# Performance work log

Measured on AMD Instinct MI355X. Metric: run time of the kernel, lower is better.

## Reference

```python
import jax, jax.numpy as jnp
import numpy as np

B, L, IN = 256, 64, 1024
SIZES = [IN, 600, 350, 200, 180]  # comp embedding MLP sizes
E = 180                           # embedding / LSTM hidden size
# Fixed AST: root -> 3 interior nodes -> 2 leaves each; leaf j uses comps [8j, 8j+8)
LEAF_IDX = [np.arange(j * 8, (j + 1) * 8) for j in range(6)]


def _xavier(key, shape):
    fan_out, fan_in = shape[0], shape[1]
    lim = float(np.sqrt(6.0 / (fan_in + fan_out)))
    return jax.random.uniform(key, shape, jnp.float32, -lim, lim)


def setup_inputs() -> dict:
    key = jax.random.key(0)
    ks = iter(jax.random.split(key, 40))
    inp = {"ast_features": jax.random.normal(next(ks), (B, L, IN), jnp.float32)}
    # comp embedding MLP
    for i in range(4):
        inp[f"ce_w{i}"] = _xavier(next(ks), (SIZES[i + 1], SIZES[i]))
        inp[f"ce_b{i}"] = jnp.zeros((SIZES[i + 1],), jnp.float32)
    # concat layers: [2E, 200, 180]
    cc = [2 * E, 200, 180]
    for i in range(2):
        inp[f"cc_w{i}"] = _xavier(next(ks), (cc[i + 1], cc[i]))
        inp[f"cc_b{i}"] = jnp.zeros((cc[i + 1],), jnp.float32)
    rg = [E, 200, 180]
    for i in range(2):
        inp[f"rg_w{i}"] = _xavier(next(ks), (rg[i + 1], rg[i]))
        inp[f"rg_b{i}"] = jnp.zeros((rg[i + 1],), jnp.float32)
    inp["pred_w"] = _xavier(next(ks), (1, 180))
    inp["pred_b"] = jnp.zeros((1,), jnp.float32)
    # LSTMs (torch gate order i,f,g,o), input E -> hidden E
    for p in ("cl", "nl"):
        inp[f"{p}_Wih"] = _xavier(next(ks), (4 * E, E))
        inp[f"{p}_Whh"] = _xavier(next(ks), (4 * E, E))
        inp[f"{p}_bih"] = jnp.zeros((4 * E,), jnp.float32)
        inp[f"{p}_bhh"] = jnp.zeros((4 * E,), jnp.float32)
    inp["no_comps"] = _xavier(next(ks), (1, E))
    inp["no_nodes"] = _xavier(next(ks), (1, E))
    return inp


def _lstm_last_h(x, Wih, Whh, bih, bhh):
    # x: (B, T, E) -> last hidden state (B, 1, E); h0=c0=0 as in torch default
    Bx = x.shape[0]
    h0 = jnp.zeros((Bx, E), x.dtype)

    def step(carry, xt):
        h, c = carry
        g = xt @ Wih.T + h @ Whh.T + bih + bhh
        i, f, gg, o = jnp.split(g, 4, axis=-1)
        c = jax.nn.sigmoid(f) * c + jax.nn.sigmoid(i) * jnp.tanh(gg)
        h = jax.nn.sigmoid(o) * jnp.tanh(c)
        return (h, c), None

    (h, _), _ = jax.lax.scan(step, (h0, h0), jnp.swapaxes(x, 0, 1))
    return h[:, None, :]


def reference(ast_features, ce_w0, ce_b0, ce_w1, ce_b1, ce_w2, ce_b2, ce_w3, ce_b3,
              cc_w0, cc_b0, cc_w1, cc_b1, rg_w0, rg_b0, rg_w1, rg_b1,
              pred_w, pred_b, cl_Wih, cl_Whh, cl_bih, cl_bhh,
              nl_Wih, nl_Whh, nl_bih, nl_bhh, no_comps, no_nodes):
    elu = jax.nn.elu
    # comp embedding MLP (dropout = identity in eval)
    x = ast_features
    for w, b in ((ce_w0, ce_b0), (ce_w1, ce_b1), (ce_w2, ce_b2), (ce_w3, ce_b3)):
        x = elu(x @ w.T + b)
    embed = x  # (B, L, E)
    Bx = embed.shape[0]

    def concat_block(nodes_h, comps_h):
        y = jnp.concatenate((nodes_h, comps_h), axis=2)  # (B,1,2E)
        for w, b in ((cc_w0, cc_b0), (cc_w1, cc_b1)):
            y = elu(y @ w.T + b)
        return y  # (B,1,E)

    no_nodes_b = jnp.broadcast_to(no_nodes[None], (Bx, 1, E))
    no_comps_b = jnp.broadcast_to(no_comps[None], (Bx, 1, E))

    def leaf_state(idx):
        comps_h = _lstm_last_h(embed[:, idx, :], cl_Wih, cl_Whh, cl_bih, cl_bhh)
        return concat_block(no_nodes_b, comps_h)

    def interior_state(children):
        nodes_h = _lstm_last_h(jnp.concatenate(children, axis=1), nl_Wih, nl_Whh, nl_bih, nl_bhh)
        return concat_block(nodes_h, no_comps_b)

    mids = [interior_state([leaf_state(LEAF_IDX[2 * i]), leaf_state(LEAF_IDX[2 * i + 1])]) for i in range(3)]
    prog = interior_state(mids)  # (B,1,E)

    x = prog
    for w, b in ((rg_w0, rg_b0), (rg_w1, rg_b1)):
        x = elu(x @ w.T + b)
    out = x @ pred_w.T + pred_b  # (B,1,1)
    return out[:, 0, 0]
```

## Files before the change

kernel.cpp:

```cpp
#include <hip/hip_runtime.h>
#include <math.h>


typedef __attribute__((ext_vector_type(8))) short bf16x8;
typedef __attribute__((ext_vector_type(4))) float f32x4;
typedef __attribute__((ext_vector_type(4))) unsigned short us4;
typedef unsigned short ushort_t;
typedef unsigned int uint_t;

__device__ __forceinline__ float elu1(float x) { return x > 0.f ? x : expm1f(x); }
__device__ __forceinline__ float sigm(float x) { return 1.f / (1.f + expf(-x)); }

__device__ __forceinline__ ushort_t f2bf(float f) {
    union { float f; uint_t u; } v; v.f = f;
    uint_t u = v.u;
    uint_t r = u + 0x7FFFu + ((u >> 16) & 1u);
    return (ushort_t)(r >> 16);
}
__device__ __forceinline__ float bf2f(ushort_t h) {
    union { uint_t u; float f; } v; v.u = ((uint_t)h) << 16;
    return v.f;
}
__device__ __forceinline__ void split2(float x, ushort_t& hi, ushort_t& lo) {
    ushort_t h = f2bf(x);
    hi = h;
    lo = f2bf(x - bf2f(h));
}

__device__ __forceinline__ bf16x8 ld8(const ushort_t* p) { return *(const bf16x8*)p; }

__device__ __forceinline__ void load_split_f32(const float* p, bf16x8& h8, bf16x8& l8) {
    const float4* q = (const float4*)p;
    float4 a = q[0], b = q[1];
    float v[8] = {a.x, a.y, a.z, a.w, b.x, b.y, b.z, b.w};
#pragma unroll
    for (int i = 0; i < 8; ++i) {
        ushort_t h, l; split2(v[i], h, l);
        h8[i] = (short)h; l8[i] = (short)l;
    }
}

__device__ __forceinline__ void gload16(const void* g, void* l) {
    __builtin_amdgcn_global_load_lds(
        (const __attribute__((address_space(1))) unsigned int*)g,
        (__attribute__((address_space(3))) unsigned int*)l,
        16, 0, 0);
}

template <bool OUTPAIR>
__global__ __launch_bounds__(256)
void gemm_lds(const ushort_t* __restrict__ Ahi, const ushort_t* __restrict__ Alo, int lda,
              const ushort_t* __restrict__ Whi, const ushort_t* __restrict__ Wlo, int ldw,
              const float* __restrict__ bias,
              float* __restrict__ Cf, ushort_t* __restrict__ Chi, ushort_t* __restrict__ Clo,
              int ldc, int N, int Kp, int act)
{
    __shared__ ushort_t lds[4 * 4096];
    const int tid  = threadIdx.x;
    const int lane = tid & 63;
    const int wave = tid >> 6;
    const int wm = wave & 1;
    const int wn = wave >> 1;
    const int j16 = lane & 15;
    const int kq  = lane >> 4;
    const int bm = blockIdx.y * 128;
    const int bn = blockIdx.x * 128;

    const ushort_t* sbase = (wave == 0) ? Ahi : (wave == 1) ? Alo
                          : (wave == 2) ? Whi : Wlo;
    const int srow0 = (wave < 2) ? bm : bn;
    const int sld   = (wave < 2) ? lda : ldw;
    const size_t soff = (size_t)(srow0 + j16) * sld + kq * 8;
    char* const lplane = (char*)lds + wave * 8192;

    f32x4 acc[4][4] = {};

    for (int k0 = 0; k0 < Kp; k0 += 32) {
#pragma unroll
        for (int u = 0; u < 8; ++u) {
            gload16(sbase + soff + (size_t)u * 16 * sld + k0, lplane + u * 1024);
        }
        __syncthreads();

        bf16x8 ah[4], al[4], bh[4], bl[4];
#pragma unroll
        for (int i = 0; i < 4; ++i) {
            const int ta = (wm * 4 + i) * 1024 + lane * 16;
            const int tb = (wn * 4 + i) * 1024 + lane * 16;
            ah[i] = *(const bf16x8*)((const char*)lds +         ta);
            al[i] = *(const bf16x8*)((const char*)lds +  8192 + ta);
            bh[i] = *(const bf16x8*)((const char*)lds + 16384 + tb);
            bl[i] = *(const bf16x8*)((const char*)lds + 24576 + tb);
        }
#pragma unroll
        for (int ms = 0; ms < 4; ++ms)
#pragma unroll
        for (int ns = 0; ns < 4; ++ns) {
            acc[ms][ns] = __builtin_amdgcn_mfma_f32_16x16x32_bf16(ah[ms], bh[ns], acc[ms][ns], 0, 0, 0);
            acc[ms][ns] = __builtin_amdgcn_mfma_f32_16x16x32_bf16(ah[ms], bl[ns], acc[ms][ns], 0, 0, 0);
            acc[ms][ns] = __builtin_amdgcn_mfma_f32_16x16x32_bf16(al[ms], bh[ns], acc[ms][ns], 0, 0, 0);
        }
        __syncthreads();
    }

    const int rbase = kq << 2;
#pragma unroll
    for (int ms = 0; ms < 4; ++ms)
#pragma unroll
    for (int ns = 0; ns < 4; ++ns) {
        const int gc = bn + wn * 64 + ns * 16 + j16;
#pragma unroll
        for (int r = 0; r < 4; ++r) {
            const int gr = bm + wm * 64 + ms * 16 + rbase + r;
            float v = acc[ms][ns][r];
            if constexpr (OUTPAIR) {
                if (gc < ldc) {
                    float o = 0.f;
                    if (gc < N) {
                        o = v + (bias ? bias[gc] : 0.f);
                        if (act) o = elu1(o);
                    }
                    ushort_t hh, ll; split2(o, hh, ll);
                    Chi[(size_t)gr * ldc + gc] = hh;
                    Clo[(size_t)gr * ldc + gc] = ll;
                }
            } else {
                if (gc < N) {
                    float o = v + (bias ? bias[gc] : 0.f);
                    if (act) o = elu1(o);
                    Cf[(size_t)gr * N + gc] = o;
                }
            }
        }
    }
}

__global__ __launch_bounds__(256)
void gemm_mfma_f32a(const float* __restrict__ A, int lda,
                    const ushort_t* __restrict__ Whi, const ushort_t* __restrict__ Wlo, int ldw,
                    const float* __restrict__ bias,
                    ushort_t* __restrict__ Chi, ushort_t* __restrict__ Clo,
                    int ldc, int N, int Kp, int act)
{
    const int lane = threadIdx.x & 63;
    const int wave = threadIdx.x >> 6;
    const int wm = wave & 1, wn = wave >> 1;
    const int r16 = lane & 15;
    const int kb  = (lane >> 4) << 3;
    const int bm = blockIdx.y * 128 + wm * 64;
    const int bn = blockIdx.x * 128 + wn * 64;

    f32x4 acc[4][4] = {};
    size_t aoff[4];
    const ushort_t *wh[4], *wl[4];
#pragma unroll
    for (int i = 0; i < 4; ++i) {
        aoff[i] = (size_t)(bm + i * 16 + r16) * lda + kb;
        wh[i] = Whi + (size_t)(bn + i * 16 + r16) * ldw + kb;
        wl[i] = Wlo + (size_t)(bn + i * 16 + r16) * ldw + kb;
    }
    for (int k = 0; k < Kp; k += 32) {
        bf16x8 ah[4], al[4], bh[4], bl[4];
#pragma unroll
        for (int i = 0; i < 4; ++i) {
            load_split_f32(A + aoff[i] + k, ah[i], al[i]);
            bh[i] = ld8(wh[i] + k);
            bl[i] = ld8(wl[i] + k);
        }
#pragma unroll
        for (int ms = 0; ms < 4; ++ms)
#pragma unroll
        for (int ns = 0; ns < 4; ++ns) {
            acc[ms][ns] = __builtin_amdgcn_mfma_f32_16x16x32_bf16(ah[ms], bh[ns], acc[ms][ns], 0, 0, 0);
            acc[ms][ns] = __builtin_amdgcn_mfma_f32_16x16x32_bf16(ah[ms], bl[ns], acc[ms][ns], 0, 0, 0);
            acc[ms][ns] = __builtin_amdgcn_mfma_f32_16x16x32_bf16(al[ms], bh[ns], acc[ms][ns], 0, 0, 0);
        }
    }
    const int rbase = (lane >> 4) << 2;
#pragma unroll
    for (int ms = 0; ms < 4; ++ms)
#pragma unroll
    for (int ns = 0; ns < 4; ++ns) {
        const int gc = bn + ns * 16 + r16;
#pragma unroll
        for (int r = 0; r < 4; ++r) {
            const int gr = bm + ms * 16 + rbase + r;
            if (gc < ldc) {
                float o = 0.f;
                if (gc < N) {
                    o = acc[ms][ns][r] + bias[gc];
                    if (act) o = elu1(o);
                }
                ushort_t hh, ll; split2(o, hh, ll);
                Chi[(size_t)gr * ldc + gc] = hh;
                Clo[(size_t)gr * ldc + gc] = ll;
            }
        }
    }
}

__global__ void conv_w(const float* __restrict__ src, int sld, int soff,
                       int R, int C, ushort_t* __restrict__ dhi,
                       ushort_t* __restrict__ dlo, int Rp, int Cp)
{
    int idx = blockIdx.x * blockDim.x + threadIdx.x;
    if (idx >= Rp * Cp) return;
    int r = idx / Cp, c = idx - r * Cp;
    float v = (r < R && c < C) ? src[r * sld + soff + c] : 0.f;
    ushort_t h, l; split2(v, h, l);
    dhi[idx] = h; dlo[idx] = l;
}

__global__ void conv_a0(const float* __restrict__ src, ushort_t* __restrict__ dhi,
                        ushort_t* __restrict__ dlo)
{
    int idx = blockIdx.x * blockDim.x + threadIdx.x;
    if (idx >= 16384 * 256) return;
    float4 v = ((const float4*)src)[idx];
    float x[4] = {v.x, v.y, v.z, v.w};
    us4 h, l;
#pragma unroll
    for (int i = 0; i < 4; ++i) {
        ushort_t hh, ll; split2(x[i], hh, ll);
        h[i] = hh; l[i] = ll;
    }
    ((us4*)dhi)[idx] = h;
    ((us4*)dlo)[idx] = l;
}

__global__ void lstm_gate(ushort_t* __restrict__ h_hi, ushort_t* __restrict__ h_lo,
                          float* __restrict__ c,
                          const float* __restrict__ G, const float* __restrict__ XW,
                          int rows, int T, int t)
{
    int idx = blockIdx.x * blockDim.x + threadIdx.x;
    if (idx >= rows * 180) return;
    int n = idx / 180, e = idx - n * 180;
    const float* xw = XW + ((size_t)n * T + t) * 720;
    float gi = xw[e], gf = xw[e + 180], gg = xw[e + 360], go = xw[e + 540];
    if (G) {
        const float* g = G + (size_t)n * 720;
        gi += g[e]; gf += g[e + 180]; gg += g[e + 360]; go += g[e + 540];
    }
    float cv = sigm(gf) * c[idx] + sigm(gi) * tanhf(gg);
    c[idx] = cv;
    float hv = sigm(go) * tanhf(cv);
    ushort_t hh, ll; split2(hv, hh, ll);
    h_hi[(size_t)n * 192 + e] = hh;
    h_lo[(size_t)n * 192 + e] = ll;
}

__global__ void gather_leaf_bf(const ushort_t* __restrict__ ehi, const ushort_t* __restrict__ elo,
                               ushort_t* __restrict__ xhi, ushort_t* __restrict__ xlo)
{
    int idx = blockIdx.x * blockDim.x + threadIdx.x;
    if (idx >= 12288 * 192) return;
    int r = idx / 192, e = idx - r * 192;
    int t = r & 7, nb = r >> 3;
    int b = nb & 255, j = nb >> 8;
    int s = (b * 64 + 8 * j + t) * 192 + e;
    xhi[idx] = ehi[s];
    xlo[idx] = elo[s];
}

__global__ void gather_mid_bf(const ushort_t* __restrict__ shi, const ushort_t* __restrict__ slo,
                              ushort_t* __restrict__ dhi, ushort_t* __restrict__ dlo)
{
    int idx = blockIdx.x * blockDim.x + threadIdx.x;
    if (idx >= 1536 * 192) return;
    int r = idx / 192, e = idx - r * 192;
    int t = r & 1, m = r >> 1;
    int b = m & 255, i = m >> 8;
    int s = ((2 * i + t) * 256 + b) * 192 + e;
    dhi[idx] = shi[s];
    dlo[idx] = slo[s];
}

__global__ void gather_root_bf(const ushort_t* __restrict__ shi, const ushort_t* __restrict__ slo,
                               ushort_t* __restrict__ dhi, ushort_t* __restrict__ dlo)
{
    int idx = blockIdx.x * blockDim.x + threadIdx.x;
    if (idx >= 768 * 192) return;
    int r = idx / 192, e = idx - r * 192;
    int b = r / 3, t = r - b * 3;
    int s = (t * 256 + b) * 192 + e;
    dhi[idx] = shi[s];
    dlo[idx] = slo[s];
}

__global__ void bias_prep(const float* __restrict__ cl_bih, const float* __restrict__ cl_bhh,
                          const float* __restrict__ nl_bih, const float* __restrict__ nl_bhh,
                          const float* __restrict__ cc_w0, const float* __restrict__ cc_b0,
                          const float* __restrict__ no_nodes, const float* __restrict__ no_comps,
                          float* __restrict__ clb, float* __restrict__ nlb,
                          float* __restrict__ b1, float* __restrict__ b2)
{
    int tid = blockIdx.x * blockDim.x + threadIdx.x;
    if (tid < 720) {
        clb[tid] = cl_bih[tid] + cl_bhh[tid];
    } else if (tid < 1440) {
        int o = tid - 720;
        nlb[o] = nl_bih[o] + nl_bhh[o];
    } else if (tid < 1640) {
        int o = tid - 1440;
        float s = cc_b0[o];
        for (int e = 0; e < 180; ++e) s = fmaf(no_nodes[e], cc_w0[o * 360 + e], s);
        b1[o] = s;
    } else if (tid < 1840) {
        int o = tid - 1640;
        float s = cc_b0[o];
        for (int e = 0; e < 180; ++e) s = fmaf(no_comps[e], cc_w0[o * 360 + 180 + e], s);
        b2[o] = s;
    }
}

__global__ void pred_kernel(const float* __restrict__ x, const float* __restrict__ pw,
                            const float* __restrict__ pb, float* __restrict__ out)
{
    int b = blockIdx.x * blockDim.x + threadIdx.x;
    if (b >= 256) return;
    float s = pb[0];
#pragma unroll 4
    for (int e = 0; e < 180; ++e) s = fmaf(x[b * 180 + e], pw[e], s);
    out[b] = s;
}

extern "C" void kernel_launch(void* const* d_in, const int* in_sizes, int n_in,
                              void* d_out, int out_size, void* d_ws, size_t ws_size,
                              hipStream_t stream)
{
    const float* ast    = (const float*)d_in[0];
    const float* ce_w0  = (const float*)d_in[1];
    const float* ce_b0  = (const float*)d_in[2];
    const float* ce_w1  = (const float*)d_in[3];
    const float* ce_b1  = (const float*)d_in[4];
    const float* ce_w2  = (const float*)d_in[5];
    const float* ce_b2  = (const float*)d_in[6];
    const float* ce_w3  = (const float*)d_in[7];
    const float* ce_b3  = (const float*)d_in[8];
    const float* cc_w0  = (const float*)d_in[9];
    const float* cc_b0  = (const float*)d_in[10];
    const float* cc_w1  = (const float*)d_in[11];
    const float* cc_b1  = (const float*)d_in[12];
    const float* rg_w0  = (const float*)d_in[13];
    const float* rg_b0  = (const float*)d_in[14];
    const float* rg_w1  = (const float*)d_in[15];
    const float* rg_b1  = (const float*)d_in[16];
    const float* pred_w = (const float*)d_in[17];
    const float* pred_b = (const float*)d_in[18];
    const float* cl_Wih = (const float*)d_in[19];
    const float* cl_Whh = (const float*)d_in[20];
    const float* cl_bih = (const float*)d_in[21];
    const float* cl_bhh = (const float*)d_in[22];
    const float* nl_Wih = (const float*)d_in[23];
    const float* nl_Whh = (const float*)d_in[24];
    const float* nl_bih = (const float*)d_in[25];
    const float* nl_bhh = (const float*)d_in[26];
    const float* no_comps = (const float*)d_in[27];
    const float* no_nodes = (const float*)d_in[28];
    float* out = (float*)d_out;

    char* ws = (char*)d_ws;

    const size_t Z1SZ = 39845888;
    const size_t WTSZ = 7560192;
    const bool pre = ws_size >= (size_t)67108864 + Z1SZ + WTSZ + 8192;
    const size_t z0sz = pre ? 67108864 : 35651584;

    char* Z0 = ws;
    char* Z1 = ws + z0sz;
    char* WT = Z1 + Z1SZ;
    char* BI = WT + WTSZ;

    ushort_t* A0hi = (ushort_t*)Z0;
    ushort_t* A0lo = (ushort_t*)(Z0 + 33554432);
    ushort_t* A2hi = (ushort_t*)Z0;
    ushort_t* A2lo = (ushort_t*)(Z0 + 11534336);
    ushort_t* EMhi = (ushort_t*)Z0;
    ushort_t* EMlo = (ushort_t*)(Z0 + 6291456);
    float*    XWl  = (float*)Z0;

    ushort_t* A1hi = (ushort_t*)Z1;
    ushort_t* A1lo = (ushort_t*)(Z1 + 19922944);
    ushort_t* A3hi = (ushort_t*)Z1;
    ushort_t* A3lo = (ushort_t*)(Z1 + 7340032);
    ushort_t* XGhi = (ushort_t*)Z1;
    ushort_t* XGlo = (ushort_t*)(Z1 + 4718592);
    char* S = Z1 + 9437184;

    ushort_t* hl_hi = (ushort_t*)(S);
    ushort_t* hl_lo = (ushort_t*)(S + 589824);
    float*    c_l   = (float*)(S + 1179648);
    float*    G     = (float*)(S + 2285568);
    ushort_t* ls_hi = (ushort_t*)(S + 6709248);
    ushort_t* ls_lo = (ushort_t*)(S + 7299072);
    ushort_t* y2_hi = (ushort_t*)(S + 7888896);
    ushort_t* y2_lo = (ushort_t*)(S + 8577024);
    ushort_t* x2_hi = (ushort_t*)(S + 9265152);
    ushort_t* x2_lo = (ushort_t*)(S + 9854976);
    float*    XW2   = (float*)(S + 10444800);
    ushort_t* hm_hi = (ushort_t*)(S + 14868480);
    ushort_t* hm_lo = (ushort_t*)(S + 15163392);
    float*    c_m   = (float*)(S + 15458304);
    ushort_t* ms_hi = (ushort_t*)(S + 16011264);
    ushort_t* ms_lo = (ushort_t*)(S + 16306176);
    ushort_t* x3_hi = (ushort_t*)(S + 16601088);
    ushort_t* x3_lo = (ushort_t*)(S + 16896000);
    float*    XW3   = (float*)(S + 17190912);
    ushort_t* hr_hi = (ushort_t*)(S + 19402752);
    ushort_t* hr_lo = (ushort_t*)(S + 19501056);
    float*    c_r   = (float*)(S + 19599360);
    ushort_t* pg_hi = (ushort_t*)(S + 19783680);
    ushort_t* pg_lo = (ushort_t*)(S + 19881984);
    ushort_t* r2_hi = (ushort_t*)(S + 19980288);
    ushort_t* r2_lo = (ushort_t*)(S + 20094976);
    float*    r180  = (float*)(S + 20209664);

    ushort_t* w0hi  = (ushort_t*)(WT);
    ushort_t* w0lo  = (ushort_t*)(WT + 1310720);
    ushort_t* w1hi  = (ushort_t*)(WT + 2621440);
    ushort_t* w1lo  = (ushort_t*)(WT + 3088384);
    ushort_t* w2hi  = (ushort_t*)(WT + 3555328);
    ushort_t* w2lo  = (ushort_t*)(WT + 3735552);
    ushort_t* w3hi  = (ushort_t*)(WT + 3915776);
    ushort_t* w3lo  = (ushort_t*)(WT + 4030464);
    ushort_t* wiC_h = (ushort_t*)(WT + 4145152);
    ushort_t* wiC_l = (ushort_t*)(WT + 4440064);
    ushort_t* whC_h = (ushort_t*)(WT + 4734976);
    ushort_t* whC_l = (ushort_t*)(WT + 5029888);
    ushort_t* wiN_h = (ushort_t*)(WT + 5324800);
    ushort_t* wiN_l = (ushort_t*)(WT + 5619712);
    ushort_t* whN_h = (ushort_t*)(WT + 5914624);
    ushort_t* whN_l = (ushort_t*)(WT + 6209536);
    ushort_t* c0L_h = (ushort_t*)(WT + 6504448);
    ushort_t* c0L_l = (ushort_t*)(WT + 6602752);
    ushort_t* c0I_h = (ushort_t*)(WT + 6701056);
    ushort_t* c0I_l = (ushort_t*)(WT + 6799360);
    ushort_t* c1_h  = (ushort_t*)(WT + 6897664);
    ushort_t* c1_l  = (ushort_t*)(WT + 7012352);
    ushort_t* rg0_h = (ushort_t*)(WT + 7127040);
    ushort_t* rg0_l = (ushort_t*)(WT + 7225344);
    ushort_t* rg1_h = (ushort_t*)(WT + 7323648);
    ushort_t* rg1_l = (ushort_t*)(WT + 7438336);

    float* clb = (float*)BI;
    float* nlb = (float*)(BI + 2880);
    float* b1  = (float*)(BI + 5760);
    float* b2  = (float*)(BI + 6560);

    if (pre)
        conv_a0<<<16384, 256, 0, stream>>>(ast, A0hi, A0lo);
    conv_w<<<(640*1024 + 255)/256, 256, 0, stream>>>(ce_w0, 1024, 0, 600, 1024, w0hi, w0lo, 640, 1024);
    conv_w<<<(384*608 + 255)/256, 256, 0, stream>>>(ce_w1, 600, 0, 350, 600, w1hi, w1lo, 384, 608);
    conv_w<<<(256*352 + 255)/256, 256, 0, stream>>>(ce_w2, 350, 0, 200, 350, w2hi, w2lo, 256, 352);
    conv_w<<<(256*224 + 255)/256, 256, 0, stream>>>(ce_w3, 200, 0, 180, 200, w3hi, w3lo, 256, 224);
    conv_w<<<(768*192 + 255)/256, 256, 0, stream>>>(cl_Wih, 180, 0, 720, 180, wiC_h, wiC_l, 768, 192);
    conv_w<<<(768*192 + 255)/256, 256, 0, stream>>>(cl_Whh, 180, 0, 720, 180, whC_h, whC_l, 768, 192);
    conv_w<<<(768*192 + 255)/256, 256, 0, stream>>>(nl_Wih, 180, 0, 720, 180, wiN_h, wiN_l, 768, 192);
    conv_w<<<(768*192 + 255)/256, 256, 0, stream>>>(nl_Whh, 180, 0, 720, 180, whN_h, whN_l, 768, 192);
    conv_w<<<(256*192 + 255)/256, 256, 0, stream>>>(cc_w0, 360, 180, 200, 180, c0L_h, c0L_l, 256, 192);
    conv_w<<<(256*192 + 255)/256, 256, 0, stream>>>(cc_w0, 360, 0, 200, 180, c0I_h, c0I_l, 256, 192);
    conv_w<<<(256*224 + 255)/256, 256, 0, stream>>>(cc_w1, 200, 0, 180, 200, c1_h, c1_l, 256, 224);
    conv_w<<<(256*192 + 255)/256, 256, 0, stream>>>(rg_w0, 180, 0, 200, 180, rg0_h, rg0_l, 256, 192);
    conv_w<<<(256*224 + 255)/256, 256, 0, stream>>>(rg_w1, 200, 0, 180, 200, rg1_h, rg1_l, 256, 224);
    bias_prep<<<(1840 + 255)/256, 256, 0, stream>>>(
        cl_bih, cl_bhh, nl_bih, nl_bhh, cc_w0, cc_b0, no_nodes, no_comps,
        clb, nlb, b1, b2);

    dim3 blk(256);

    if (pre)
        gemm_lds<true><<<dim3(5, 128), blk, 0, stream>>>(
            A0hi, A0lo, 1024, w0hi, w0lo, 1024, ce_b0,
            nullptr, A1hi, A1lo, 608, 600, 1024, 1);
    else
        gemm_mfma_f32a<<<dim3(5, 128), blk, 0, stream>>>(
            ast, 1024, w0hi, w0lo, 1024, ce_b0,
            A1hi, A1lo, 608, 600, 1024, 1);
    gemm_lds<true><<<dim3(3, 128), blk, 0, stream>>>(
        A1hi, A1lo, 608, w1hi, w1lo, 608, ce_b1,
        nullptr, A2hi, A2lo, 352, 350, 608, 1);
    gemm_lds<true><<<dim3(2, 128), blk, 0, stream>>>(
        A2hi, A2lo, 352, w2hi, w2lo, 352, ce_b2,
        nullptr, A3hi, A3lo, 224, 200, 352, 1);
    gemm_lds<true><<<dim3(2, 128), blk, 0, stream>>>(
        A3hi, A3lo, 224, w3hi, w3lo, 224, ce_b3,
        nullptr, EMhi, EMlo, 192, 180, 224, 1);

    gather_leaf_bf<<<(12288*192 + 255)/256, 256, 0, stream>>>(EMhi, EMlo, XGhi, XGlo);
    gemm_lds<false><<<dim3(6, 96), blk, 0, stream>>>(
        XGhi, XGlo, 192, wiC_h, wiC_l, 192, clb,
        XWl, nullptr, nullptr, 0, 720, 192, 0);
    hipMemsetAsync(S, 0, 2285568, stream);
    for (int t = 0; t < 8; ++t) {
        if (t > 0)
            gemm_lds<false><<<dim3(6, 12), blk, 0, stream>>>(
                hl_hi, hl_lo, 192, whC_h, whC_l, 192, nullptr,
                G, nullptr, nullptr, 0, 720, 192, 0);
        lstm_gate<<<(1536*180 + 255)/256, 256, 0, stream>>>(
            hl_hi, hl_lo, c_l, t ? G : nullptr, XWl, 1536, 8, t);
    }
    gemm_lds<true><<<dim3(2, 12), blk, 0, stream>>>(
        hl_hi, hl_lo, 192, c0L_h, c0L_l, 192, b1,
        nullptr, y2_hi, y2_lo, 224, 200, 192, 1);
    gemm_lds<true><<<dim3(2, 12), blk, 0, stream>>>(
        y2_hi, y2_lo, 224, c1_h, c1_l, 224, cc_b1,
        nullptr, ls_hi, ls_lo, 192, 180, 224, 1);

    gather_mid_bf<<<(1536*192 + 255)/256, 256, 0, stream>>>(ls_hi, ls_lo, x2_hi, x2_lo);
    gemm_lds<false><<<dim3(6, 12), blk, 0, stream>>>(
        x2_hi, x2_lo, 192, wiN_h, wiN_l, 192, nlb,
        XW2, nullptr, nullptr, 0, 720, 192, 0);
    hipMemsetAsync(S + 14868480, 0, 1142784, stream);
    for (int t = 0; t < 2; ++t) {
        if (t > 0)
            gemm_lds<false><<<dim3(6, 6), blk, 0, stream>>>(
                hm_hi, hm_lo, 192, whN_h, whN_l, 192, nullptr,
                G, nullptr, nullptr, 0, 720, 192, 0);
        lstm_gate<<<(768*180 + 255)/256, 256, 0, stream>>>(
            hm_hi, hm_lo, c_m, t ? G : nullptr, XW2, 768, 2, t);
    }
    gemm_lds<true><<<dim3(2, 6), blk, 0, stream>>>(
        hm_hi, hm_lo, 192, c0I_h, c0I_l, 192, b2,
        nullptr, y2_hi, y2_lo, 224, 200, 192, 1);
    gemm_lds<true><<<dim3(2, 6), blk, 0, stream>>>(
        y2_hi, y2_lo, 224, c1_h, c1_l, 224, cc_b1,
        nullptr, ms_hi, ms_lo, 192, 180, 224, 1);

    gather_root_bf<<<(768*192 + 255)/256, 256, 0, stream>>>(ms_hi, ms_lo, x3_hi, x3_lo);
    gemm_lds<false><<<dim3(6, 6), blk, 0, stream>>>(
        x3_hi, x3_lo, 192, wiN_h, wiN_l, 192, nlb,
        XW3, nullptr, nullptr, 0, 720, 192, 0);
    hipMemsetAsync(S + 19402752, 0, 380928, stream);
    for (int t = 0; t < 3; ++t) {
        if (t > 0)
            gemm_lds<false><<<dim3(6, 2), blk, 0, stream>>>(
                hr_hi, hr_lo, 192, whN_h, whN_l, 192, nullptr,
                G, nullptr, nullptr, 0, 720, 192, 0);
        lstm_gate<<<(256*180 + 255)/256, 256, 0, stream>>>(
            hr_hi, hr_lo, c_r, t ? G : nullptr, XW3, 256, 3, t);
    }
    gemm_lds<true><<<dim3(2, 2), blk, 0, stream>>>(
        hr_hi, hr_lo, 192, c0I_h, c0I_l, 192, b2,
        nullptr, y2_hi, y2_lo, 224, 200, 192, 1);
    gemm_lds<true><<<dim3(2, 2), blk, 0, stream>>>(
        y2_hi, y2_lo, 224, c1_h, c1_l, 224, cc_b1,
        nullptr, pg_hi, pg_lo, 192, 180, 224, 1);

    gemm_lds<true><<<dim3(2, 2), blk, 0, stream>>>(
        pg_hi, pg_lo, 192, rg0_h, rg0_l, 192, rg_b0,
        nullptr, r2_hi, r2_lo, 224, 200, 192, 1);
    gemm_lds<false><<<dim3(2, 2), blk, 0, stream>>>(
        r2_hi, r2_lo, 224, rg1_h, rg1_l, 224, rg_b1,
        r180, nullptr, nullptr, 0, 180, 224, 1);
    pred_kernel<<<1, 256, 0, stream>>>(r180, pred_w, pred_b, out);
}
```

Measured before the change: 1.066 ms.

## Double-buffer LDS in split-bf16 GEMM, remap workgroups, fuse weight prep launches

The GEMM kernel now uses a 64KB dynamic LDS double buffer, so the global-to-LDS loads for the next K tile are issued while the MFMAs on the current tile run, and one barrier per iteration is removed. Workgroup IDs are remapped in groups of 8 when the grid size allows it, which changes which tiles run on which part of the GPU and may affect cache locality. The thirteen weight conversion kernels, the bias prep kernel and the three memsets are merged into a single prep_all launch to cut launch overhead. Doubling the LDS per block may reduce occupancy.

```diff
diff --git a/kernel.cpp b/kernel.cpp
--- a/kernel.cpp
+++ b/kernel.cpp
@@ -55,7 +55,7 @@
               float* __restrict__ Cf, ushort_t* __restrict__ Chi, ushort_t* __restrict__ Clo,
               int ldc, int N, int Kp, int act)
 {
-    __shared__ ushort_t lds[4 * 4096];
+    extern __shared__ char smem[];
     const int tid  = threadIdx.x;
     const int lane = tid & 63;
     const int wave = tid >> 6;
@@ -63,34 +63,49 @@
     const int wn = wave >> 1;
     const int j16 = lane & 15;
     const int kq  = lane >> 4;
-    const int bm = blockIdx.y * 128;
-    const int bn = blockIdx.x * 128;
+
+    const int gx = gridDim.x;
+    const int nwg = gx * gridDim.y;
+    int wg = blockIdx.y * gx + blockIdx.x;
+    if ((nwg & 7) == 0) {
+        const int cpx = nwg >> 3;
+        wg = (wg & 7) * cpx + (wg >> 3);
+    }
+    const int bm = (wg / gx) * 128;
+    const int bn = (wg % gx) * 128;
 
     const ushort_t* sbase = (wave == 0) ? Ahi : (wave == 1) ? Alo
                           : (wave == 2) ? Whi : Wlo;
     const int srow0 = (wave < 2) ? bm : bn;
     const int sld   = (wave < 2) ? lda : ldw;
     const size_t soff = (size_t)(srow0 + j16) * sld + kq * 8;
-    char* const lplane = (char*)lds + wave * 8192;
+    const int lp = wave * 8192;
 
     f32x4 acc[4][4] = {};
 
+#pragma unroll
+    for (int u = 0; u < 8; ++u)
+        gload16(sbase + soff + (size_t)u * 16 * sld, smem + lp + u * 1024);
+    __syncthreads();
+
+    int cur = 0;
     for (int k0 = 0; k0 < Kp; k0 += 32) {
-#pragma unroll
-        for (int u = 0; u < 8; ++u) {
-            gload16(sbase + soff + (size_t)u * 16 * sld + k0, lplane + u * 1024);
-        }
-        __syncthreads();
-
+        if (k0 + 32 < Kp) {
+            char* nb = smem + ((cur ^ 1) << 15) + lp;
+#pragma unroll
+            for (int u = 0; u < 8; ++u)
+                gload16(sbase + soff + (size_t)u * 16 * sld + k0 + 32, nb + u * 1024);
+        }
+        const char* cb = smem + (cur << 15);
         bf16x8 ah[4], al[4], bh[4], bl[4];
 #pragma unroll
         for (int i = 0; i < 4; ++i) {
             const int ta = (wm * 4 + i) * 1024 + lane * 16;
             const int tb = (wn * 4 + i) * 1024 + lane * 16;
-            ah[i] = *(const bf16x8*)((const char*)lds +         ta);
-            al[i] = *(const bf16x8*)((const char*)lds +  8192 + ta);
-            bh[i] = *(const bf16x8*)((const char*)lds + 16384 + tb);
-            bl[i] = *(const bf16x8*)((const char*)lds + 24576 + tb);
+            ah[i] = *(const bf16x8*)(cb +         ta);
+            al[i] = *(const bf16x8*)(cb +  8192 + ta);
+            bh[i] = *(const bf16x8*)(cb + 16384 + tb);
+            bl[i] = *(const bf16x8*)(cb + 24576 + tb);
         }
 #pragma unroll
         for (int ms = 0; ms < 4; ++ms)
@@ -101,6 +116,7 @@
             acc[ms][ns] = __builtin_amdgcn_mfma_f32_16x16x32_bf16(al[ms], bh[ns], acc[ms][ns], 0, 0, 0);
         }
         __syncthreads();
+        cur ^= 1;
     }
 
     const int rbase = kq << 2;
@@ -199,18 +215,6 @@
     }
 }
 
-__global__ void conv_w(const float* __restrict__ src, int sld, int soff,
-                       int R, int C, ushort_t* __restrict__ dhi,
-                       ushort_t* __restrict__ dlo, int Rp, int Cp)
-{
-    int idx = blockIdx.x * blockDim.x + threadIdx.x;
-    if (idx >= Rp * Cp) return;
-    int r = idx / Cp, c = idx - r * Cp;
-    float v = (r < R && c < C) ? src[r * sld + soff + c] : 0.f;
-    ushort_t h, l; split2(v, h, l);
-    dhi[idx] = h; dlo[idx] = l;
-}
-
 __global__ void conv_a0(const float* __restrict__ src, ushort_t* __restrict__ dhi,
                         ushort_t* __restrict__ dlo)
 {
@@ -226,6 +230,80 @@
     }
     ((us4*)dhi)[idx] = h;
     ((us4*)dlo)[idx] = l;
+}
+
+__device__ __forceinline__ bool do_conv(int idx, int base, int cnt, int Cp,
+    const float* __restrict__ src, int sld, int soff, int R, int C,
+    ushort_t* __restrict__ dhi, ushort_t* __restrict__ dlo)
+{
+    if (idx >= base + cnt) return false;
+    int k = idx - base;
+    int r = k / Cp, c = k - r * Cp;
+    float v = (r < R && c < C) ? src[r * sld + soff + c] : 0.f;
+    ushort_t h, l; split2(v, h, l);
+    dhi[k] = h; dlo[k] = l;
+    return true;
+}
+
+__global__ void prep_all(
+    const float* __restrict__ ce_w0, const float* __restrict__ ce_w1,
+    const float* __restrict__ ce_w2, const float* __restrict__ ce_w3,
+    const float* __restrict__ cl_Wih, const float* __restrict__ cl_Whh,
+    const float* __restrict__ nl_Wih, const float* __restrict__ nl_Whh,
+    const float* __restrict__ cc_w0, const float* __restrict__ cc_w1,
+    const float* __restrict__ rg_w0, const float* __restrict__ rg_w1,
+    const float* __restrict__ cl_bih, const float* __restrict__ cl_bhh,
+    const float* __restrict__ nl_bih, const float* __restrict__ nl_bhh,
+    const float* __restrict__ cc_b0,
+    const float* __restrict__ no_nodes, const float* __restrict__ no_comps,
+    ushort_t* w0hi, ushort_t* w0lo, ushort_t* w1hi, ushort_t* w1lo,
+    ushort_t* w2hi, ushort_t* w2lo, ushort_t* w3hi, ushort_t* w3lo,
+    ushort_t* wiC_h, ushort_t* wiC_l, ushort_t* whC_h, ushort_t* whC_l,
+    ushort_t* wiN_h, ushort_t* wiN_l, ushort_t* whN_h, ushort_t* whN_l,
+    ushort_t* c0L_h, ushort_t* c0L_l, ushort_t* c0I_h, ushort_t* c0I_l,
+    ushort_t* c1_h, ushort_t* c1_l, ushort_t* rg0_h, ushort_t* rg0_l,
+    ushort_t* rg1_h, ushort_t* rg1_l,
+    float* clb, float* nlb, float* b1, float* b2,
+    char* S)
+{
+    int idx = blockIdx.x * blockDim.x + threadIdx.x;
+    if (do_conv(idx,       0, 655360, 1024, ce_w0, 1024, 0, 600, 1024, w0hi, w0lo)) return;
+    if (do_conv(idx,  655360, 233472,  608, ce_w1,  600, 0, 350,  600, w1hi, w1lo)) return;
+    if (do_conv(idx,  888832,  90112,  352, ce_w2,  350, 0, 200,  350, w2hi, w2lo)) return;
+    if (do_conv(idx,  978944,  57344,  224, ce_w3,  200, 0, 180,  200, w3hi, w3lo)) return;
+    if (do_conv(idx, 1036288, 147456,  192, cl_Wih, 180, 0, 720,  180, wiC_h, wiC_l)) return;
+    if (do_conv(idx, 1183744, 147456,  192, cl_Whh, 180, 0, 720,  180, whC_h, whC_l)) return;
+    if (do_conv(idx, 1331200, 147456,  192, nl_Wih, 180, 0, 720,  180, wiN_h, wiN_l)) return;
+    if (do_conv(idx, 1478656, 147456,  192, nl_Whh, 180, 0, 720,  180, whN_h, whN_l)) return;
+    if (do_conv(idx, 1626112,  49152,  192, cc_w0,  360, 180, 200, 180, c0L_h, c0L_l)) return;
+    if (do_conv(idx, 1675264,  49152,  192, cc_w0,  360, 0, 200,  180, c0I_h, c0I_l)) return;
+    if (do_conv(idx, 1724416,  57344,  224, cc_w1,  200, 0, 180,  200, c1_h, c1_l)) return;
+    if (do_conv(idx, 1781760,  49152,  192, rg_w0,  180, 0, 200,  180, rg0_h, rg0_l)) return;
+    if (do_conv(idx, 1830912,  57344,  224, rg_w1,  200, 0, 180,  200, rg1_h, rg1_l)) return;
+    if (idx < 1890096) {
+        int tid = idx - 1888256;
+        if (tid < 720) {
+            clb[tid] = cl_bih[tid] + cl_bhh[tid];
+        } else if (tid < 1440) {
+            int o = tid - 720;
+            nlb[o] = nl_bih[o] + nl_bhh[o];
+        } else if (tid < 1640) {
+            int o = tid - 1440;
+            float s = cc_b0[o];
+            for (int e = 0; e < 180; ++e) s = fmaf(no_nodes[e], cc_w0[o * 360 + e], s);
+            b1[o] = s;
+        } else if (tid < 1840) {
+            int o = tid - 1640;
+            float s = cc_b0[o];
+            for (int e = 0; e < 180; ++e) s = fmaf(no_comps[e], cc_w0[o * 360 + 180 + e], s);
+            b2[o] = s;
+        }
+        return;
+    }
+    float4 z = make_float4(0.f, 0.f, 0.f, 0.f);
+    if (idx < 2032944) { ((float4*)(S))[idx - 1890096] = z; return; }
+    if (idx < 2104368) { ((float4*)(S + 14868480))[idx - 2032944] = z; return; }
+    if (idx < 2128176) { ((float4*)(S + 19402752))[idx - 2104368] = z; return; }
 }
 
 __global__ void lstm_gate(ushort_t* __restrict__ h_hi, ushort_t* __restrict__ h_lo,
@@ -286,32 +364,6 @@
     int s = (t * 256 + b) * 192 + e;
     dhi[idx] = shi[s];
     dlo[idx] = slo[s];
-}
-
-__global__ void bias_prep(const float* __restrict__ cl_bih, const float* __restrict__ cl_bhh,
-                          const float* __restrict__ nl_bih, const float* __restrict__ nl_bhh,
-                          const float* __restrict__ cc_w0, const float* __restrict__ cc_b0,
-                          const float* __restrict__ no_nodes, const float* __restrict__ no_comps,
-                          float* __restrict__ clb, float* __restrict__ nlb,
-                          float* __restrict__ b1, float* __restrict__ b2)
-{
-    int tid = blockIdx.x * blockDim.x + threadIdx.x;
-    if (tid < 720) {
-        clb[tid] = cl_bih[tid] + cl_bhh[tid];
-    } else if (tid < 1440) {
-        int o = tid - 720;
-        nlb[o] = nl_bih[o] + nl_bhh[o];
-    } else if (tid < 1640) {
-        int o = tid - 1440;
-        float s = cc_b0[o];
-        for (int e = 0; e < 180; ++e) s = fmaf(no_nodes[e], cc_w0[o * 360 + e], s);
-        b1[o] = s;
-    } else if (tid < 1840) {
-        int o = tid - 1640;
-        float s = cc_b0[o];
-        for (int e = 0; e < 180; ++e) s = fmaf(no_comps[e], cc_w0[o * 360 + 180 + e], s);
-        b2[o] = s;
-    }
 }
 
 __global__ void pred_kernel(const float* __restrict__ x, const float* __restrict__ pw,
@@ -450,107 +502,97 @@
 
     if (pre)
         conv_a0<<<16384, 256, 0, stream>>>(ast, A0hi, A0lo);
-    conv_w<<<(640*1024 + 255)/256, 256, 0, stream>>>(ce_w0, 1024, 0, 600, 1024, w0hi, w0lo, 640, 1024);
-    conv_w<<<(384*608 + 255)/256, 256, 0, stream>>>(ce_w1, 600, 0, 350, 600, w1hi, w1lo, 384, 608);
-    conv_w<<<(256*352 + 255)/256, 256, 0, stream>>>(ce_w2, 350, 0, 200, 350, w2hi, w2lo, 256, 352);
-    conv_w<<<(256*224 + 255)/256, 256, 0, stream>>>(ce_w3, 200, 0, 180, 200, w3hi, w3lo, 256, 224);
-    conv_w<<<(768*192 + 255)/256, 256, 0, stream>>>(cl_Wih, 180, 0, 720, 180, wiC_h, wiC_l, 768, 192);
-    conv_w<<<(768*192 + 255)/256, 256, 0, stream>>>(cl_Whh, 180, 0, 720, 180, whC_h, whC_l, 768, 192);
-    conv_w<<<(768*192 + 255)/256, 256, 0, stream>>>(nl_Wih, 180, 0, 720, 180, wiN_h, wiN_l, 768, 192);
-    conv_w<<<(768*192 + 255)/256, 256, 0, stream>>>(nl_Whh, 180, 0, 720, 180, whN_h, whN_l, 768, 192);
-    conv_w<<<(256*192 + 255)/256, 256, 0, stream>>>(cc_w0, 360, 180, 200, 180, c0L_h, c0L_l, 256, 192);
-    conv_w<<<(256*192 + 255)/256, 256, 0, stream>>>(cc_w0, 360, 0, 200, 180, c0I_h, c0I_l, 256, 192);
-    conv_w<<<(256*224 + 255)/256, 256, 0, stream>>>(cc_w1, 200, 0, 180, 200, c1_h, c1_l, 256, 224);
-    conv_w<<<(256*192 + 255)/256, 256, 0, stream>>>(rg_w0, 180, 0, 200, 180, rg0_h, rg0_l, 256, 192);
-    conv_w<<<(256*224 + 255)/256, 256, 0, stream>>>(rg_w1, 200, 0, 180, 200, rg1_h, rg1_l, 256, 224);
-    bias_prep<<<(1840 + 255)/256, 256, 0, stream>>>(
-        cl_bih, cl_bhh, nl_bih, nl_bhh, cc_w0, cc_b0, no_nodes, no_comps,
-        clb, nlb, b1, b2);
+    prep_all<<<(2128176 + 255) / 256, 256, 0, stream>>>(
+        ce_w0, ce_w1, ce_w2, ce_w3, cl_Wih, cl_Whh, nl_Wih, nl_Whh,
+        cc_w0, cc_w1, rg_w0, rg_w1,
+        cl_bih, cl_bhh, nl_bih, nl_bhh, cc_b0, no_nodes, no_comps,
+        w0hi, w0lo, w1hi, w1lo, w2hi, w2lo, w3hi, w3lo,
+        wiC_h, wiC_l, whC_h, whC_l, wiN_h, wiN_l, whN_h, whN_l,
+        c0L_h, c0L_l, c0I_h, c0I_l, c1_h, c1_l, rg0_h, rg0_l, rg1_h, rg1_l,
+        clb, nlb, b1, b2, S);
 
     dim3 blk(256);
+    const int SH = 65536;
 
     if (pre)
-        gemm_lds<true><<<dim3(5, 128), blk, 0, stream>>>(
+        gemm_lds<true><<<dim3(5, 128), blk, SH, stream>>>(
             A0hi, A0lo, 1024, w0hi, w0lo, 1024, ce_b0,
             nullptr, A1hi, A1lo, 608, 600, 1024, 1);
     else
         gemm_mfma_f32a<<<dim3(5, 128), blk, 0, stream>>>(
             ast, 1024, w0hi, w0lo, 1024, ce_b0,
             A1hi, A1lo, 608, 600, 1024, 1);
-    gemm_lds<true><<<dim3(3, 128), blk, 0, stream>>>(
+    gemm_lds<true><<<dim3(3, 128), blk, SH, stream>>>(
         A1hi, A1lo, 608, w1hi, w1lo, 608, ce_b1,
         nullptr, A2hi, A2lo, 352, 350, 608, 1);
-    gemm_lds<true><<<dim3(2, 128), blk, 0, stream>>>(
+    gemm_lds<true><<<dim3(2, 128), blk, SH, stream>>>(
         A2hi, A2lo, 352, w2hi, w2lo, 352, ce_b2,
         nullptr, A3hi, A3lo, 224, 200, 352, 1);
-    gemm_lds<true><<<dim3(2, 128), blk, 0, stream>>>(
+    gemm_lds<true><<<dim3(2, 128), blk, SH, stream>>>(
         A3hi, A3lo, 224, w3hi, w3lo, 224, ce_b3,
         nullptr, EMhi, EMlo, 192, 180, 224, 1);
 
     gather_leaf_bf<<<(12288*192 + 255)/256, 256, 0, stream>>>(EMhi, EMlo, XGhi, XGlo);
-    gemm_lds<false><<<dim3(6, 96), blk, 0, stream>>>(
+    gemm_lds<false><<<dim3(6, 96), blk, SH, stream>>>(
         XGhi, XGlo, 192, wiC_h, wiC_l, 192, clb,
         XWl, nullptr, nullptr, 0, 720, 192, 0);
-    hipMemsetAsync(S, 0, 2285568, stream);
     for (int t = 0; t < 8; ++t) {
         if (t > 0)
-            gemm_lds<false><<<dim3(6, 12), blk, 0, stream>>>(
+            gemm_lds<false><<<dim3(6, 12), blk, SH, stream>>>(
                 hl_hi, hl_lo, 192, whC_h, whC_l, 192, nullptr,
                 G, nullptr, nullptr, 0, 720, 192, 0);
         lstm_gate<<<(1536*180 + 255)/256, 256, 0, stream>>>(
             hl_hi, hl_lo, c_l, t ? G : nullptr, XWl, 1536, 8, t);
     }
-    gemm_lds<true><<<dim3(2, 12), blk, 0, stream>>>(
+    gemm_lds<true><<<dim3(2, 12), blk, SH, stream>>>(
         hl_hi, hl_lo, 192, c0L_h, c0L_l, 192, b1,
         nullptr, y2_hi, y2_lo, 224, 200, 192, 1);
-    gemm_lds<true><<<dim3(2, 12), blk, 0, stream>>>(
+    gemm_lds<true><<<dim3(2, 12), blk, SH, stream>>>(
         y2_hi, y2_lo, 224, c1_h, c1_l, 224, cc_b1,
         nullptr, ls_hi, ls_lo, 192, 180, 224, 1);
 
     gather_mid_bf<<<(1536*192 + 255)/256, 256, 0, stream>>>(ls_hi, ls_lo, x2_hi, x2_lo);
-    gemm_lds<false><<<dim3(6, 12), blk, 0, stream>>>(
+    gemm_lds<false><<<dim3(6, 12), blk, SH, stream>>>(
         x2_hi, x2_lo, 192, wiN_h, wiN_l, 192, nlb,
         XW2, nullptr, nullptr, 0, 720, 192, 0);
-    hipMemsetAsync(S + 14868480, 0, 1142784, stream);
     for (int t = 0; t < 2; ++t) {
         if (t > 0)
-            gemm_lds<false><<<dim3(6, 6), blk, 0, stream>>>(
+            gemm_lds<false><<<dim3(6, 6), blk, SH, stream>>>(
                 hm_hi, hm_lo, 192, whN_h, whN_l, 192, nullptr,
                 G, nullptr, nullptr, 0, 720, 192, 0);
         lstm_gate<<<(768*180 + 255)/256, 256, 0, stream>>>(
             hm_hi, hm_lo, c_m, t ? G : nullptr, XW2, 768, 2, t);
     }
-    gemm_lds<true><<<dim3(2, 6), blk, 0, stream>>>(
+    gemm_lds<true><<<dim3(2, 6), blk, SH, stream>>>(
         hm_hi, hm_lo, 192, c0I_h, c0I_l, 192, b2,
         nullptr, y2_hi, y2_lo, 224, 200, 192, 1);
-    gemm_lds<true><<<dim3(2, 6), blk, 0, stream>>>(
+    gemm_lds<true><<<dim3(2, 6), blk, SH, stream>>>(
         y2_hi, y2_lo, 224, c1_h, c1_l, 224, cc_b1,
         nullptr, ms_hi, ms_lo, 192, 180, 224, 1);
 
     gather_root_bf<<<(768*192 + 255)/256, 256, 0, stream>>>(ms_hi, ms_lo, x3_hi, x3_lo);
-    gemm_lds<false><<<dim3(6, 6), blk, 0, stream>>>(
+    gemm_lds<false><<<dim3(6, 6), blk, SH, stream>>>(
         x3_hi, x3_lo, 192, wiN_h, wiN_l, 192, nlb,
         XW3, nullptr, nullptr, 0, 720, 192, 0);
-    hipMemsetAsync(S + 19402752, 0, 380928, stream);
     for (int t = 0; t < 3; ++t) {
         if (t > 0)
-            gemm_lds<false><<<dim3(6, 2), blk, 0, stream>>>(
+            gemm_lds<false><<<dim3(6, 2), blk, SH, stream>>>(
                 hr_hi, hr_lo, 192, whN_h, whN_l, 192, nullptr,
                 G, nullptr, nullptr, 0, 720, 192, 0);
         lstm_gate<<<(256*180 + 255)/256, 256, 0, stream>>>(
             hr_hi, hr_lo, c_r, t ? G : nullptr, XW3, 256, 3, t);
     }
-    gemm_lds<true><<<dim3(2, 2), blk, 0, stream>>>(
+    gemm_lds<true><<<dim3(2, 2), blk, SH, stream>>>(
         hr_hi, hr_lo, 192, c0I_h, c0I_l, 192, b2,
         nullptr, y2_hi, y2_lo, 224, 200, 192, 1);
-    gemm_lds<true><<<dim3(2, 2), blk, 0, stream>>>(
+    gemm_lds<true><<<dim3(2, 2), blk, SH, stream>>>(
         y2_hi, y2_lo, 224, c1_h, c1_l, 224, cc_b1,
         nullptr, pg_hi, pg_lo, 192, 180, 224, 1);
 
-    gemm_lds<true><<<dim3(2, 2), blk, 0, stream>>>(
+    gemm_lds<true><<<dim3(2, 2), blk, SH, stream>>>(
         pg_hi, pg_lo, 192, rg0_h, rg0_l, 192, rg_b0,
         nullptr, r2_hi, r2_lo, 224, 200, 192, 1);
-    gemm_lds<false><<<dim3(2, 2), blk, 0, stream>>>(
+    gemm_lds<false><<<dim3(2, 2), blk, SH, stream>>>(
         r2_hi, r2_lo, 224, rg1_h, rg1_l, 224, rg_b1,
         r180, nullptr, nullptr, 0, 180, 224, 1);
     pred_kernel<<<1, 256, 0, stream>>>(r180, pred_w, pred_b, out);
```

Result: faster. 996.8 us (-6.5%).
